# Performance work log

Hardware: AMD Instinct MI355X
Metric: run time of the kernel (lower is better)

Reference implementation:

```python
import jax, jax.numpy as jnp
import numpy as np

BATCH, SEQ, HIDDEN = 8, 4096, 1024

def setup_inputs() -> dict:
    key = jax.random.key(0)
    hidden_states = jax.random.normal(key, (BATCH, SEQ, HIDDEN), dtype=jnp.float32)
    return {"hidden_states": hidden_states}

def reference(hidden_states) -> jnp.ndarray:
    # FFT along the sequence axis with orthonormal normalization (1/sqrt(N)),
    # then keep only the real part (FNet-style Fourier token mixing).
    fft_out = jnp.fft.fft(hidden_states, axis=1, norm="ortho")
    return jnp.real(fft_out).astype(hidden_states.dtype)
```

## Files before the change

### kernel.cpp

```cpp
#include <hip/hip_runtime.h>
#include <hip/hip_fp16.h>


static constexpr int SEQ = 4096;
static constexpr int HID = 1024;

struct alignas(8) h2x2 { __half2 a, b; };

typedef float nv4 __attribute__((ext_vector_type(4)));

__device__ __forceinline__ int rev4_3(int r) {
    return ((r & 3) << 4) | (r & 12) | ((r >> 4) & 3);
}


__device__ __forceinline__ void fft8(float* xr, float* xi) {
    const float C = 0.70710678118654752f;
    float ar[8], ai[8];
    ar[0] = xr[0] + xr[4];  ai[0] = xi[0] + xi[4];
    ar[1] = xr[0] - xr[4];  ai[1] = xi[0] - xi[4];
    ar[2] = xr[2] + xr[6];  ai[2] = xi[2] + xi[6];
    ar[3] = xr[2] - xr[6];  ai[3] = xi[2] - xi[6];
    ar[4] = xr[1] + xr[5];  ai[4] = xi[1] + xi[5];
    ar[5] = xr[1] - xr[5];  ai[5] = xi[1] - xi[5];
    ar[6] = xr[3] + xr[7];  ai[6] = xi[3] + xi[7];
    ar[7] = xr[3] - xr[7];  ai[7] = xi[3] - xi[7];
    float br[8], bi[8];
    br[0] = ar[0] + ar[2];  bi[0] = ai[0] + ai[2];
    br[2] = ar[0] - ar[2];  bi[2] = ai[0] - ai[2];
    br[1] = ar[1] + ai[3];  bi[1] = ai[1] - ar[3];
    br[3] = ar[1] - ai[3];  bi[3] = ai[1] + ar[3];
    br[4] = ar[4] + ar[6];  bi[4] = ai[4] + ai[6];
    br[6] = ar[4] - ar[6];  bi[6] = ai[4] - ai[6];
    br[5] = ar[5] + ai[7];  bi[5] = ai[5] - ar[7];
    br[7] = ar[5] - ai[7];  bi[7] = ai[5] + ar[7];
    const float t0r = br[4],                 t0i = bi[4];
    const float t1r = C * (br[5] + bi[5]),   t1i = C * (bi[5] - br[5]);
    const float t2r = bi[6],                 t2i = -br[6];
    const float t3r = C * (bi[7] - br[7]),   t3i = -C * (br[7] + bi[7]);
    xr[0] = br[0] + t0r;  xi[0] = bi[0] + t0i;
    xr[4] = br[0] - t0r;  xi[4] = bi[0] - t0i;
    xr[1] = br[1] + t1r;  xi[1] = bi[1] + t1i;
    xr[5] = br[1] - t1r;  xi[5] = bi[1] - t1i;
    xr[2] = br[2] + t2r;  xi[2] = bi[2] + t2i;
    xr[6] = br[2] - t2r;  xi[6] = bi[2] - t2i;
    xr[3] = br[3] + t3r;  xi[3] = bi[3] + t3i;
    xr[7] = br[3] - t3r;  xi[7] = bi[3] - t3i;
}

__device__ __forceinline__ void twiddle_chain(float* xr, float* xi,
                                              const float wc, const float ws) {
    float cr = wc, ci = ws;
    #pragma unroll
    for (int k = 1; k < 8; ++k) {
        const float tr = xr[k] * cr - xi[k] * ci;
        xi[k] = xr[k] * ci + xi[k] * cr;
        xr[k] = tr;
        if (k < 7) {
            const float nr = cr * wc - ci * ws;
            const float ni = cr * ws + ci * wc;
            cr = nr;  ci = ni;
        }
    }
}


__global__ __launch_bounds__(512, 4) void fft_pass1_x2(const float* __restrict__ x,
                                                       __half2* __restrict__ u) {
    __shared__ float4 zs[64 * 65];
    const int t  = threadIdx.x;
    const int pc = blockIdx.x & 3;
    const int n2 = (blockIdx.x >> 2) & 63;
    const int b  = blockIdx.x >> 8;
    const int c  = t & 63;
    const int q  = t >> 6;

    const float* xb = x + (size_t)b * SEQ * HID + (size_t)(pc * 256 + 4 * c);
    nv4 raw[8];
    #pragma unroll
    for (int a = 0; a < 8; ++a)
        raw[a] = __builtin_nontemporal_load(
            (const nv4*)(xb + (size_t)(n2 + 64 * (8 * a + q)) * HID));

    float wq_s, wq_c;
    __sincosf(-0.09817477042468103f * (float)q, &wq_s, &wq_c);

    float fr0[8], fi0[8], fr1[8], fi1[8];
    #pragma unroll
    for (int a = 0; a < 8; ++a) { fr0[a] = raw[a].x; fi0[a] = raw[a].y; }
    fft8(fr0, fi0);
    twiddle_chain(fr0, fi0, wq_c, wq_s);
    #pragma unroll
    for (int a = 0; a < 8; ++a) { fr1[a] = raw[a].z; fi1[a] = raw[a].w; }
    fft8(fr1, fi1);
    twiddle_chain(fr1, fi1, wq_c, wq_s);

    #pragma unroll
    for (int k = 0; k < 8; ++k)
        zs[(k * 8 + q) * 65 + c] = make_float4(fr0[k], fi0[k], fr1[k], fi1[k]);
    __syncthreads();
    float4 rw[8];
    #pragma unroll
    for (int r = 0; r < 8; ++r) rw[r] = zs[(q * 8 + r) * 65 + c];

    #pragma unroll
    for (int a = 0; a < 8; ++a) { fr0[a] = rw[a].x; fi0[a] = rw[a].y; }
    fft8(fr0, fi0);
    #pragma unroll
    for (int a = 0; a < 8; ++a) { fr1[a] = rw[a].z; fi1[a] = rw[a].w; }
    fft8(fr1, fi1);

    const float tw = -1.5339807878856412e-3f;
    float w0c, w0s, wsc, wss;
    __sincosf(tw * (float)(n2 * q), &w0s, &w0c);
    __sincosf(tw * (float)(n2 * 8), &wss, &wsc);
    const float sc = 0.015625f;
    w0c *= sc;  w0s *= sc;
    __half2* ub = u + (size_t)b * SEQ * 512 + (size_t)(64 * q + n2) * 512 + pc * 128 + 2 * c;
    #pragma unroll
    for (int kh = 0; kh < 8; ++kh) {
        h2x2 o;
        o.a = __floats2half2_rn(fr0[kh] * w0c - fi0[kh] * w0s,
                                fr0[kh] * w0s + fi0[kh] * w0c);
        o.b = __floats2half2_rn(fr1[kh] * w0c - fi1[kh] * w0s,
                                fr1[kh] * w0s + fi1[kh] * w0c);
        *(h2x2*)(ub + (size_t)kh * (512 * 512)) = o;
        if (kh < 7) {
            const float nc = w0c * wsc - w0s * wss;
            const float ns = w0c * wss + w0s * wsc;
            w0c = nc;  w0s = ns;
        }
    }
}

__global__ __launch_bounds__(512, 4) void fft_pass2_x2(const __half2* __restrict__ u,
                                                       float* __restrict__ out) {
    __shared__ float4 vs[128 * 33];
    const int t   = threadIdx.x;
    const int b   = blockIdx.x >> 8;
    const int idx = blockIdx.x & 255;
    const __half2* ub = u   + (size_t)b * SEQ * 512;
    float*         ob = out + (size_t)b * SEQ * HID;
    const float scale = 0.5f;
    float fr0[8], fi0[8], fr1[8], fi1[8];

    if (idx < 248) {
        const int k1 = 1 + (idx >> 3);
        const int pc = idx & 7;
        const int ab = t >> 8;
        const int q  = (t >> 5) & 7;
        const int c  = t & 31;
        const int k1sel = ab ? 64 - k1 : k1;
        const int p  = pc * 64 + 2 * c;
        const __half2* up = ub + (size_t)(64 * k1sel) * 512 + p;
        h2x2 raw[8];
        #pragma unroll
        for (int a = 0; a < 8; ++a)
            raw[a] = *(const h2x2*)(up + (size_t)(8 * a + q) * 512);

        float wq_s, wq_c;
        __sincosf(-0.09817477042468103f * (float)q, &wq_s, &wq_c);
        #pragma unroll
        for (int a = 0; a < 8; ++a) {
            const float2 v = __half22float2(raw[a].a);
            fr0[a] = v.x;  fi0[a] = v.y;
        }
        fft8(fr0, fi0);
        twiddle_chain(fr0, fi0, wq_c, wq_s);
        #pragma unroll
        for (int a = 0; a < 8; ++a) {
            const float2 v = __half22float2(raw[a].b);
            fr1[a] = v.x;  fi1[a] = v.y;
        }
        fft8(fr1, fi1);
        twiddle_chain(fr1, fi1, wq_c, wq_s);

        const int base = ab * 64;
        #pragma unroll
        for (int k = 0; k < 8; ++k)
            vs[(base + k * 8 + q) * 33 + c] = make_float4(fr0[k], fi0[k], fr1[k], fi1[k]);
        __syncthreads();
        float4 rw[8];
        #pragma unroll
        for (int r = 0; r < 8; ++r) rw[r] = vs[(base + q * 8 + r) * 33 + c];
        #pragma unroll
        for (int a = 0; a < 8; ++a) { fr0[a] = rw[a].x; fi0[a] = rw[a].y; }
        fft8(fr0, fi0);
        #pragma unroll
        for (int a = 0; a < 8; ++a) { fr1[a] = rw[a].z; fi1[a] = rw[a].w; }
        fft8(fr1, fi1);
        __syncthreads();
        #pragma unroll
        for (int k = 0; k < 8; ++k)
            vs[(base + k * 8 + q) * 33 + c] = make_float4(fr0[k], fi0[k], fr1[k], fi1[k]);
        __syncthreads();

        float* op = ob + (size_t)k1sel * HID + (size_t)(pc * 128 + 4 * c);
        #pragma unroll
        for (int kh = 0; kh < 8; ++kh) {
            const float4 pv = vs[((64 - base) + (7 - kh) * 8 + (7 - q)) * 33 + c];
            const int k2 = q + 8 * kh;
            nv4 o;
            o.x = (fr0[kh] + pv.x) * scale;
            o.y = (fi0[kh] + pv.y) * scale;
            o.z = (fr1[kh] + pv.z) * scale;
            o.w = (fi1[kh] + pv.w) * scale;
            __builtin_nontemporal_store(o, (nv4*)(op + (size_t)(64 * k2) * HID));
        }
    } else {
        const int s  = idx - 248;
        const int k1 = (s >> 2) * 32;
        const int pc = s & 3;
        const int q  = t >> 6;
        const int c  = t & 63;
        const int p  = pc * 128 + 2 * c;
        const __half2* up = ub + (size_t)(64 * k1) * 512 + p;
        h2x2 raw[8];
        #pragma unroll
        for (int a = 0; a < 8; ++a)
            raw[a] = *(const h2x2*)(up + (size_t)(8 * a + q) * 512);

        float wq_s, wq_c;
        __sincosf(-0.09817477042468103f * (float)q, &wq_s, &wq_c);
        #pragma unroll
        for (int a = 0; a < 8; ++a) {
            const float2 v = __half22float2(raw[a].a);
            fr0[a] = v.x;  fi0[a] = v.y;
        }
        fft8(fr0, fi0);
        twiddle_chain(fr0, fi0, wq_c, wq_s);
        #pragma unroll
        for (int a = 0; a < 8; ++a) {
            const float2 v = __half22float2(raw[a].b);
            fr1[a] = v.x;  fi1[a] = v.y;
        }
        fft8(fr1, fi1);
        twiddle_chain(fr1, fi1, wq_c, wq_s);

        #pragma unroll
        for (int k = 0; k < 8; ++k)
            vs[(k * 8 + q) * 65 + c] = make_float4(fr0[k], fi0[k], fr1[k], fi1[k]);
        __syncthreads();
        float4 rw[8];
        #pragma unroll
        for (int r = 0; r < 8; ++r) rw[r] = vs[(q * 8 + r) * 65 + c];
        #pragma unroll
        for (int a = 0; a < 8; ++a) { fr0[a] = rw[a].x; fi0[a] = rw[a].y; }
        fft8(fr0, fi0);
        #pragma unroll
        for (int a = 0; a < 8; ++a) { fr1[a] = rw[a].z; fi1[a] = rw[a].w; }
        fft8(fr1, fi1);
        __syncthreads();
        #pragma unroll
        for (int k = 0; k < 8; ++k)
            vs[(k * 8 + q) * 65 + c] = make_float4(fr0[k], fi0[k], fr1[k], fi1[k]);
        __syncthreads();

        const int q2 = (k1 == 0) ? ((8 - q) & 7) : (7 - q);
        float* op = ob + (size_t)k1 * HID + (size_t)(pc * 256 + 4 * c);
        #pragma unroll
        for (int kh = 0; kh < 8; ++kh) {
            const int kh2 = (k1 == 0 && q == 0) ? ((8 - kh) & 7) : (7 - kh);
            const float4 pv = vs[(kh2 * 8 + q2) * 65 + c];
            const int k2 = q + 8 * kh;
            nv4 o;
            o.x = (fr0[kh] + pv.x) * scale;
            o.y = (fi0[kh] + pv.y) * scale;
            o.z = (fr1[kh] + pv.z) * scale;
            o.w = (fi1[kh] + pv.w) * scale;
            __builtin_nontemporal_store(o, (nv4*)(op + (size_t)(64 * k2) * HID));
        }
    }
}


template <int MC>
__device__ __forceinline__ void fft64_lds(float* re, float* im, int off, int stride, int mbase) {
    #pragma unroll
    for (int s = 0; s < 3; ++s) {
        const int L = 1 << (2 * s);
        const float ang = -6.283185307179586f / (float)(4 * L);
        #pragma unroll
        for (int mi = 0; mi < MC; ++mi) {
            const int m  = mbase + mi;
            const int j  = m & (L - 1);
            const int i0 = ((m >> (2 * s)) << (2 * s + 2)) + j;
            const int a0 = (i0        ) * stride + off;
            const int a1 = (i0 +     L) * stride + off;
            const int a2 = (i0 + 2 * L) * stride + off;
            const int a3 = (i0 + 3 * L) * stride + off;
            const float e0x = re[a0], e0y = im[a0];
            const float e1x = re[a1], e1y = im[a1];
            const float e2x = re[a2], e2y = im[a2];
            const float e3x = re[a3], e3y = im[a3];
            float w1s, w1c;
            __sincosf(ang * (float)j, &w1s, &w1c);
            const float w2c = w1c * w1c - w1s * w1s, w2s = 2.f * w1c * w1s;
            const float w3c = w2c * w1c - w2s * w1s, w3s = w2c * w1s + w2s * w1c;
            const float t1x = e1x * w1c - e1y * w1s, t1y = e1x * w1s + e1y * w1c;
            const float t2x = e2x * w2c - e2y * w2s, t2y = e2x * w2s + e2y * w2c;
            const float t3x = e3x * w3c - e3y * w3s, t3y = e3x * w3s + e3y * w3c;
            const float a02x = e0x + t2x, a02y = e0y + t2y;
            const float s02x = e0x - t2x, s02y = e0y - t2y;
            const float a13x = t1x + t3x, a13y = t1y + t3y;
            const float s13x = t1x - t3x, s13y = t1y - t3y;
            re[a0] = a02x + a13x;  im[a0] = a02y + a13y;
            re[a1] = s02x + s13y;  im[a1] = s02y - s13x;
            re[a2] = a02x - a13x;  im[a2] = a02y - a13y;
            re[a3] = s02x - s13y;  im[a3] = s02y + s13x;
        }
        __syncthreads();
    }
}

__global__ __launch_bounds__(256) void fft_pass1(const float* __restrict__ x,
                                                 float* __restrict__ out) {
    __shared__ float sre[64 * 65];
    __shared__ float sim[64 * 65];
    const int t  = threadIdx.x;
    const int pc = blockIdx.x & 7;
    const int n2 = (blockIdx.x >> 3) & 63;
    const int b  = blockIdx.x >> 9;
    const float* xb = x   + (size_t)b * SEQ * HID + pc * 128;
    float*       ob = out + (size_t)b * SEQ * HID + pc * 128;

    const int c  = t & 31;
    const int r0 = t >> 5;
    #pragma unroll
    for (int i = 0; i < 8; ++i) {
        const int r  = r0 + 8 * i;
        const float4 f = *(const float4*)(xb + (size_t)(n2 + 64 * r) * HID + 4 * c);
        const int rr = rev4_3(r);
        sre[rr * 65 + 2 * c]     = f.x;  sim[rr * 65 + 2 * c]     = f.y;
        sre[rr * 65 + 2 * c + 1] = f.z;  sim[rr * 65 + 2 * c + 1] = f.w;
    }
    __syncthreads();

    fft64_lds<4>(sre, sim, t & 63, 65, 4 * (t >> 6));

    const float tw = -1.5339807878856412e-3f;
    #pragma unroll
    for (int i = 0; i < 8; ++i) {
        const int k1 = r0 + 8 * i;
        float ws, wc;
        __sincosf(tw * (float)(n2 * k1), &ws, &wc);
        const float ar = sre[k1 * 65 + 2 * c],     ai = sim[k1 * 65 + 2 * c];
        const float br = sre[k1 * 65 + 2 * c + 1], bi = sim[k1 * 65 + 2 * c + 1];
        float4 f;
        f.x = ar * wc - ai * ws;  f.y = ar * ws + ai * wc;
        f.z = br * wc - bi * ws;  f.w = br * ws + bi * wc;
        *(float4*)(ob + (size_t)(64 * n2 + k1) * HID + 4 * c) = f;
    }
}

__global__ __launch_bounds__(256) void fft_pass2(float* out) {
    __shared__ float lds[8448];
    const int t   = threadIdx.x;
    const int b   = blockIdx.x >> 9;
    const int idx = blockIdx.x & 511;
    float* ob = out + (size_t)b * SEQ * HID;
    const float scale = 1.0f / 128.0f;

    if (idx < 496) {
        const int k1 = 1 + (idx >> 4);
        const int pc = idx & 15;
        float* are = lds;          float* aim = lds + 2112;
        float* bre = lds + 4224;   float* bim = lds + 6336;
        const int c  = t & 15;
        const int rg = t >> 4;
        #pragma unroll
        for (int i = 0; i < 4; ++i) {
            const int n2 = rg + 16 * i;
            const int rr = rev4_3(n2);
            const float4 fa = *(const float4*)(ob + (size_t)(64 * n2 + k1)      * HID + pc * 64 + 4 * c);
            const float4 fb = *(const float4*)(ob + (size_t)(64 * n2 + 64 - k1) * HID + pc * 64 + 4 * c);
            are[rr * 33 + 2 * c]     = fa.x;  aim[rr * 33 + 2 * c]     = fa.y;
            are[rr * 33 + 2 * c + 1] = fa.z;  aim[rr * 33 + 2 * c + 1] = fa.w;
            bre[rr * 33 + 2 * c]     = fb.x;  bim[rr * 33 + 2 * c]     = fb.y;
            bre[rr * 33 + 2 * c + 1] = fb.z;  bim[rr * 33 + 2 * c + 1] = fb.w;
        }
        __syncthreads();

        const int lane = t & 63;
        float* fre = lds + 4224 * (lane >> 5);
        fft64_lds<4>(fre, fre + 2112, lane & 31, 33, 4 * (t >> 6));

        #pragma unroll
        for (int i = 0; i < 4; ++i) {
            const int k2 = rg + 16 * i;
            const int q  = 63 - k2;
            float4 f, g;
            f.x = (are[k2 * 33 + 2 * c]     + bre[q * 33 + 2 * c])     * scale;
            f.y = (aim[k2 * 33 + 2 * c]     + bim[q * 33 + 2 * c])     * scale;
            f.z = (are[k2 * 33 + 2 * c + 1] + bre[q * 33 + 2 * c + 1]) * scale;
            f.w = (aim[k2 * 33 + 2 * c + 1] + bim[q * 33 + 2 * c + 1]) * scale;
            *(float4*)(ob + (size_t)(k1 + 64 * k2)      * HID + pc * 64 + 4 * c) = f;
            g.x = (bre[k2 * 33 + 2 * c]     + are[q * 33 + 2 * c])     * scale;
            g.y = (bim[k2 * 33 + 2 * c]     + aim[q * 33 + 2 * c])     * scale;
            g.z = (bre[k2 * 33 + 2 * c + 1] + are[q * 33 + 2 * c + 1]) * scale;
            g.w = (bim[k2 * 33 + 2 * c + 1] + aim[q * 33 + 2 * c + 1]) * scale;
            *(float4*)(ob + (size_t)(64 - k1 + 64 * k2) * HID + pc * 64 + 4 * c) = g;
        }
    } else {
        const int s  = idx - 496;
        const int k1 = (s >> 3) * 32;
        const int pc = s & 7;
        float* sre = lds;
        float* sim = lds + 4160;
        const int c  = t & 31;
        const int rg = t >> 5;
        #pragma unroll
        for (int i = 0; i < 8; ++i) {
            const int n2 = rg + 8 * i;
            const int rr = rev4_3(n2);
            const float4 f = *(const float4*)(ob + (size_t)(64 * n2 + k1) * HID + pc * 128 + 4 * c);
            sre[rr * 65 + 2 * c]     = f.x;  sim[rr * 65 + 2 * c]     = f.y;
            sre[rr * 65 + 2 * c + 1] = f.z;  sim[rr * 65 + 2 * c + 1] = f.w;
        }
        __syncthreads();

        fft64_lds<4>(sre, sim, t & 63, 65, 4 * (t >> 6));

        #pragma unroll
        for (int i = 0; i < 8; ++i) {
            const int k2 = rg + 8 * i;
            const int q  = (k1 == 0) ? ((64 - k2) & 63) : (63 - k2);
            float4 f;
            f.x = (sre[k2 * 65 + 2 * c]     + sre[q * 65 + 2 * c])     * scale;
            f.y = (sim[k2 * 65 + 2 * c]     + sim[q * 65 + 2 * c])     * scale;
            f.z = (sre[k2 * 65 + 2 * c + 1] + sre[q * 65 + 2 * c + 1]) * scale;
            f.w = (sim[k2 * 65 + 2 * c + 1] + sim[q * 65 + 2 * c + 1]) * scale;
            *(float4*)(ob + (size_t)(k1 + 64 * k2) * HID + pc * 128 + 4 * c) = f;
        }
    }
}

extern "C" void kernel_launch(void* const* d_in, const int* in_sizes, int n_in,
                              void* d_out, int out_size, void* d_ws, size_t ws_size,
                              hipStream_t stream) {
    const float* x = (const float*)d_in[0];
    float* out = (float*)d_out;
    const size_t need = (size_t)8 * SEQ * 512 * sizeof(__half2);
    if (ws_size >= need) {
        __half2* u = (__half2*)d_ws;
        fft_pass1_x2<<<dim3(8 * 64 * 4), dim3(512), 0, stream>>>(x, u);
        fft_pass2_x2<<<dim3(8 * 256), dim3(512), 0, stream>>>(u, out);
    } else {
        fft_pass1<<<dim3(8 * 64 * 8), dim3(256), 0, stream>>>(x, out);
        fft_pass2<<<dim3(8 * 512), dim3(256), 0, stream>>>(out);
    }
}
```

Measured before the change: 240.5 us.

## Widen FFT tiles: pass1 handles 8 columns per thread, pass2 uses 1024-thread blocks

Pass 1 now loads two float4 per row, so each thread processes 8 hidden columns (4 complex pairs). It runs two fft8/transposition rounds through shared memory and writes 16-byte half2x4 stores, which halves the grid. Pass 2 moves to 1024-thread blocks covering twice the column width, with larger LDS strides. The aim is wider memory transactions and fewer blocks. In exchange, pass 1 needs more registers and an extra sync, and pass 2 needs more LDS per block, which may reduce occupancy.

```diff
diff --git a/kernel.cpp b/kernel.cpp
--- a/kernel.cpp
+++ b/kernel.cpp
@@ -5,7 +5,8 @@
 static constexpr int SEQ = 4096;
 static constexpr int HID = 1024;
 
-struct alignas(8) h2x2 { __half2 a, b; };
+struct alignas(8)  h2x2 { __half2 a, b; };
+struct alignas(16) h2x4 { h2x2 a, b; };
 
 typedef float nv4 __attribute__((ext_vector_type(4)));
 
@@ -65,93 +66,105 @@
 }
 
 
-__global__ __launch_bounds__(512, 4) void fft_pass1_x2(const float* __restrict__ x,
+__global__ __launch_bounds__(512, 4) void fft_pass1_x4(const float* __restrict__ x,
                                                        __half2* __restrict__ u) {
     __shared__ float4 zs[64 * 65];
     const int t  = threadIdx.x;
-    const int pc = blockIdx.x & 3;
-    const int n2 = (blockIdx.x >> 2) & 63;
-    const int b  = blockIdx.x >> 8;
+    const int pc = blockIdx.x & 1;
+    const int n2 = (blockIdx.x >> 1) & 63;
+    const int b  = blockIdx.x >> 7;
     const int c  = t & 63;
     const int q  = t >> 6;
 
-    const float* xb = x + (size_t)b * SEQ * HID + (size_t)(pc * 256 + 4 * c);
-    nv4 raw[8];
-    #pragma unroll
-    for (int a = 0; a < 8; ++a)
-        raw[a] = __builtin_nontemporal_load(
-            (const nv4*)(xb + (size_t)(n2 + 64 * (8 * a + q)) * HID));
+    const float* xb = x + (size_t)b * SEQ * HID + (size_t)(pc * 512 + 8 * c);
+    nv4 rawA[8], rawB[8];
+    #pragma unroll
+    for (int a = 0; a < 8; ++a) {
+        const float* rp = xb + (size_t)(n2 + 64 * (8 * a + q)) * HID;
+        rawA[a] = __builtin_nontemporal_load((const nv4*)rp);
+        rawB[a] = __builtin_nontemporal_load((const nv4*)(rp + 4));
+    }
 
     float wq_s, wq_c;
     __sincosf(-0.09817477042468103f * (float)q, &wq_s, &wq_c);
-
-    float fr0[8], fi0[8], fr1[8], fi1[8];
-    #pragma unroll
-    for (int a = 0; a < 8; ++a) { fr0[a] = raw[a].x; fi0[a] = raw[a].y; }
-    fft8(fr0, fi0);
-    twiddle_chain(fr0, fi0, wq_c, wq_s);
-    #pragma unroll
-    for (int a = 0; a < 8; ++a) { fr1[a] = raw[a].z; fi1[a] = raw[a].w; }
-    fft8(fr1, fi1);
-    twiddle_chain(fr1, fi1, wq_c, wq_s);
-
-    #pragma unroll
-    for (int k = 0; k < 8; ++k)
-        zs[(k * 8 + q) * 65 + c] = make_float4(fr0[k], fi0[k], fr1[k], fi1[k]);
-    __syncthreads();
-    float4 rw[8];
-    #pragma unroll
-    for (int r = 0; r < 8; ++r) rw[r] = zs[(q * 8 + r) * 65 + c];
-
-    #pragma unroll
-    for (int a = 0; a < 8; ++a) { fr0[a] = rw[a].x; fi0[a] = rw[a].y; }
-    fft8(fr0, fi0);
-    #pragma unroll
-    for (int a = 0; a < 8; ++a) { fr1[a] = rw[a].z; fi1[a] = rw[a].w; }
-    fft8(fr1, fi1);
-
     const float tw = -1.5339807878856412e-3f;
-    float w0c, w0s, wsc, wss;
-    __sincosf(tw * (float)(n2 * q), &w0s, &w0c);
+    float w0c0, w0s0, wsc, wss;
+    __sincosf(tw * (float)(n2 * q), &w0s0, &w0c0);
     __sincosf(tw * (float)(n2 * 8), &wss, &wsc);
     const float sc = 0.015625f;
-    w0c *= sc;  w0s *= sc;
-    __half2* ub = u + (size_t)b * SEQ * 512 + (size_t)(64 * q + n2) * 512 + pc * 128 + 2 * c;
+    w0c0 *= sc;  w0s0 *= sc;
+
+    h2x2 o0[8], o1[8];
+    #pragma unroll
+    for (int g = 0; g < 2; ++g) {
+        float fr0[8], fi0[8], fr1[8], fi1[8];
+        #pragma unroll
+        for (int a = 0; a < 8; ++a) {
+            const nv4 v = g ? rawB[a] : rawA[a];
+            fr0[a] = v.x;  fi0[a] = v.y;  fr1[a] = v.z;  fi1[a] = v.w;
+        }
+        fft8(fr0, fi0);  twiddle_chain(fr0, fi0, wq_c, wq_s);
+        fft8(fr1, fi1);  twiddle_chain(fr1, fi1, wq_c, wq_s);
+
+        #pragma unroll
+        for (int k = 0; k < 8; ++k)
+            zs[(k * 8 + q) * 65 + c] = make_float4(fr0[k], fi0[k], fr1[k], fi1[k]);
+        __syncthreads();
+        float4 rw[8];
+        #pragma unroll
+        for (int r = 0; r < 8; ++r) rw[r] = zs[(q * 8 + r) * 65 + c];
+        __syncthreads();
+
+        #pragma unroll
+        for (int a = 0; a < 8; ++a) { fr0[a] = rw[a].x; fi0[a] = rw[a].y; }
+        fft8(fr0, fi0);
+        #pragma unroll
+        for (int a = 0; a < 8; ++a) { fr1[a] = rw[a].z; fi1[a] = rw[a].w; }
+        fft8(fr1, fi1);
+
+        float w0c = w0c0, w0s = w0s0;
+        h2x2* oo = g ? o1 : o0;
+        #pragma unroll
+        for (int kh = 0; kh < 8; ++kh) {
+            oo[kh].a = __floats2half2_rn(fr0[kh] * w0c - fi0[kh] * w0s,
+                                         fr0[kh] * w0s + fi0[kh] * w0c);
+            oo[kh].b = __floats2half2_rn(fr1[kh] * w0c - fi1[kh] * w0s,
+                                         fr1[kh] * w0s + fi1[kh] * w0c);
+            if (kh < 7) {
+                const float nc = w0c * wsc - w0s * wss;
+                const float ns = w0c * wss + w0s * wsc;
+                w0c = nc;  w0s = ns;
+            }
+        }
+    }
+
+    __half2* ub = u + (size_t)b * SEQ * 512 + (size_t)(64 * q + n2) * 512 + pc * 256 + 4 * c;
     #pragma unroll
     for (int kh = 0; kh < 8; ++kh) {
-        h2x2 o;
-        o.a = __floats2half2_rn(fr0[kh] * w0c - fi0[kh] * w0s,
-                                fr0[kh] * w0s + fi0[kh] * w0c);
-        o.b = __floats2half2_rn(fr1[kh] * w0c - fi1[kh] * w0s,
-                                fr1[kh] * w0s + fi1[kh] * w0c);
-        *(h2x2*)(ub + (size_t)kh * (512 * 512)) = o;
-        if (kh < 7) {
-            const float nc = w0c * wsc - w0s * wss;
-            const float ns = w0c * wss + w0s * wsc;
-            w0c = nc;  w0s = ns;
-        }
-    }
-}
-
-__global__ __launch_bounds__(512, 4) void fft_pass2_x2(const __half2* __restrict__ u,
-                                                       float* __restrict__ out) {
-    __shared__ float4 vs[128 * 33];
+        h2x4 o;  o.a = o0[kh];  o.b = o1[kh];
+        *(h2x4*)(ub + (size_t)kh * (512 * 512)) = o;
+    }
+}
+
+__global__ __launch_bounds__(1024, 4) void fft_pass2_x4(const __half2* __restrict__ u,
+                                                        float* __restrict__ out) {
+    __shared__ float4 vs[8320];
     const int t   = threadIdx.x;
-    const int b   = blockIdx.x >> 8;
-    const int idx = blockIdx.x & 255;
+    const int b   = blockIdx.x >> 7;
+    const int idx = blockIdx.x & 127;
     const __half2* ub = u   + (size_t)b * SEQ * 512;
     float*         ob = out + (size_t)b * SEQ * HID;
     const float scale = 0.5f;
     float fr0[8], fi0[8], fr1[8], fi1[8];
 
-    if (idx < 248) {
-        const int k1 = 1 + (idx >> 3);
-        const int pc = idx & 7;
-        const int ab = t >> 8;
-        const int q  = (t >> 5) & 7;
-        const int c  = t & 31;
+    if (idx < 124) {
+        const int k1 = 1 + (idx >> 2);
+        const int pc = idx & 3;
+        const int ab = t >> 9;
+        const int q  = (t >> 6) & 7;
+        const int c  = t & 63;
         const int k1sel = ab ? 64 - k1 : k1;
-        const int p  = pc * 64 + 2 * c;
+        const int p  = pc * 128 + 2 * c;
         const __half2* up = ub + (size_t)(64 * k1sel) * 512 + p;
         h2x2 raw[8];
         #pragma unroll
@@ -178,11 +191,11 @@
         const int base = ab * 64;
         #pragma unroll
         for (int k = 0; k < 8; ++k)
-            vs[(base + k * 8 + q) * 33 + c] = make_float4(fr0[k], fi0[k], fr1[k], fi1[k]);
+            vs[(base + k * 8 + q) * 65 + c] = make_float4(fr0[k], fi0[k], fr1[k], fi1[k]);
         __syncthreads();
         float4 rw[8];
         #pragma unroll
-        for (int r = 0; r < 8; ++r) rw[r] = vs[(base + q * 8 + r) * 33 + c];
+        for (int r = 0; r < 8; ++r) rw[r] = vs[(base + q * 8 + r) * 65 + c];
         #pragma unroll
         for (int a = 0; a < 8; ++a) { fr0[a] = rw[a].x; fi0[a] = rw[a].y; }
         fft8(fr0, fi0);
@@ -192,13 +205,13 @@
         __syncthreads();
         #pragma unroll
         for (int k = 0; k < 8; ++k)
-            vs[(base + k * 8 + q) * 33 + c] = make_float4(fr0[k], fi0[k], fr1[k], fi1[k]);
-        __syncthreads();
-
-        float* op = ob + (size_t)k1sel * HID + (size_t)(pc * 128 + 4 * c);
+            vs[(base + k * 8 + q) * 65 + c] = make_float4(fr0[k], fi0[k], fr1[k], fi1[k]);
+        __syncthreads();
+
+        float* op = ob + (size_t)k1sel * HID + (size_t)(pc * 256 + 4 * c);
         #pragma unroll
         for (int kh = 0; kh < 8; ++kh) {
-            const float4 pv = vs[((64 - base) + (7 - kh) * 8 + (7 - q)) * 33 + c];
+            const float4 pv = vs[((64 - base) + (7 - kh) * 8 + (7 - q)) * 65 + c];
             const int k2 = q + 8 * kh;
             nv4 o;
             o.x = (fr0[kh] + pv.x) * scale;
@@ -208,12 +221,12 @@
             __builtin_nontemporal_store(o, (nv4*)(op + (size_t)(64 * k2) * HID));
         }
     } else {
-        const int s  = idx - 248;
-        const int k1 = (s >> 2) * 32;
-        const int pc = s & 3;
-        const int q  = t >> 6;
-        const int c  = t & 63;
-        const int p  = pc * 128 + 2 * c;
+        const int s  = idx - 124;
+        const int k1 = (s >> 1) * 32;
+        const int pc = s & 1;
+        const int q  = t >> 7;
+        const int c  = t & 127;
+        const int p  = pc * 256 + 2 * c;
         const __half2* up = ub + (size_t)(64 * k1) * 512 + p;
         h2x2 raw[8];
         #pragma unroll
@@ -239,11 +252,11 @@
 
         #pragma unroll
         for (int k = 0; k < 8; ++k)
-            vs[(k * 8 + q) * 65 + c] = make_float4(fr0[k], fi0[k], fr1[k], fi1[k]);
+            vs[(k * 8 + q) * 129 + c] = make_float4(fr0[k], fi0[k], fr1[k], fi1[k]);
         __syncthreads();
         float4 rw[8];
         #pragma unroll
-        for (int r = 0; r < 8; ++r) rw[r] = vs[(q * 8 + r) * 65 + c];
+        for (int r = 0; r < 8; ++r) rw[r] = vs[(q * 8 + r) * 129 + c];
         #pragma unroll
         for (int a = 0; a < 8; ++a) { fr0[a] = rw[a].x; fi0[a] = rw[a].y; }
         fft8(fr0, fi0);
@@ -253,15 +266,15 @@
         __syncthreads();
         #pragma unroll
         for (int k = 0; k < 8; ++k)
-            vs[(k * 8 + q) * 65 + c] = make_float4(fr0[k], fi0[k], fr1[k], fi1[k]);
+            vs[(k * 8 + q) * 129 + c] = make_float4(fr0[k], fi0[k], fr1[k], fi1[k]);
         __syncthreads();
 
         const int q2 = (k1 == 0) ? ((8 - q) & 7) : (7 - q);
-        float* op = ob + (size_t)k1 * HID + (size_t)(pc * 256 + 4 * c);
+        float* op = ob + (size_t)k1 * HID + (size_t)(pc * 512 + 4 * c);
         #pragma unroll
         for (int kh = 0; kh < 8; ++kh) {
             const int kh2 = (k1 == 0 && q == 0) ? ((8 - kh) & 7) : (7 - kh);
-            const float4 pv = vs[(kh2 * 8 + q2) * 65 + c];
+            const float4 pv = vs[(kh2 * 8 + q2) * 129 + c];
             const int k2 = q + 8 * kh;
             nv4 o;
             o.x = (fr0[kh] + pv.x) * scale;
@@ -443,8 +456,8 @@
     const size_t need = (size_t)8 * SEQ * 512 * sizeof(__half2);
     if (ws_size >= need) {
         __half2* u = (__half2*)d_ws;
-        fft_pass1_x2<<<dim3(8 * 64 * 4), dim3(512), 0, stream>>>(x, u);
-        fft_pass2_x2<<<dim3(8 * 256), dim3(512), 0, stream>>>(u, out);
+        fft_pass1_x4<<<dim3(8 * 64 * 2), dim3(512), 0, stream>>>(x, u);
+        fft_pass2_x4<<<dim3(8 * 128), dim3(1024), 0, stream>>>(u, out);
     } else {
         fft_pass1<<<dim3(8 * 64 * 8), dim3(256), 0, stream>>>(x, out);
         fft_pass2<<<dim3(8 * 512), dim3(256), 0, stream>>>(out);
```

Result: slower. 273.3 us (+13.6%).
